# Kernel tuning notes

Measured on AMD Instinct MI355X. Metric: run time of the kernel, lower is better.

## Reference

```python
import jax, jax.numpy as jnp
import numpy as np

B = 2048
C = 128000


def setup_inputs() -> dict:
    key = jax.random.key(0)
    k1, k2 = jax.random.split(key)
    logits = jax.random.normal(k1, (B, C), dtype=jnp.float32)
    y = jax.random.randint(k2, (B,), 0, C, dtype=jnp.int64)
    return {"logits": logits, "y": y}


def reference(logits, y):
    # top-2 logits/indices per row (replaces full descending sort in torch)
    _, top2_idx = jax.lax.top_k(logits, 2)  # [B, 2]
    # if the argmax equals the true label, use the runner-up class
    target = jnp.where(top2_idx[:, 0] == y, top2_idx[:, 1], top2_idx[:, 0])  # [B]
    first = jnp.take_along_axis(logits, target[:, None], axis=1)[:, 0]  # [B]
    # NOTE: faithful to original: subtract the *logit* value (not exp(first))
    second = jnp.log(jnp.exp(logits).sum(axis=1) - first)
    return first - second
```

## Files before the change

### kernel.cpp

```cpp
#include <hip/hip_runtime.h>
#include <math.h>

#define THREADS 256
#define WAVES (THREADS / 64)

__global__ __launch_bounds__(THREADS) void Fitness_29918742183959_kernel(
    const float* __restrict__ logits,
    const int*   __restrict__ y,
    float*       __restrict__ out,
    int C)
{
    const int row = blockIdx.x;
    const int tid = threadIdx.x;
    const float4* rowp =
        reinterpret_cast<const float4*>(logits + (size_t)row * (size_t)C);
    const int n4 = C >> 2;

    float s0 = 0.f, s1 = 0.f, s2 = 0.f, s3 = 0.f;
    float v1 = -INFINITY, v2 = -INFINITY;
    int   i1 = -1,        i2 = -1;

    for (int i = tid; i < n4; i += THREADS) {
        float4 v = rowp[i];
        const int base = i << 2;
        s0 += __expf(v.x);
        s1 += __expf(v.y);
        s2 += __expf(v.z);
        s3 += __expf(v.w);
        if (v.x > v2) { if (v.x > v1) { v2 = v1; i2 = i1; v1 = v.x; i1 = base;     } else { v2 = v.x; i2 = base;     } }
        if (v.y > v2) { if (v.y > v1) { v2 = v1; i2 = i1; v1 = v.y; i1 = base + 1; } else { v2 = v.y; i2 = base + 1; } }
        if (v.z > v2) { if (v.z > v1) { v2 = v1; i2 = i1; v1 = v.z; i1 = base + 2; } else { v2 = v.z; i2 = base + 2; } }
        if (v.w > v2) { if (v.w > v1) { v2 = v1; i2 = i1; v1 = v.w; i1 = base + 3; } else { v2 = v.w; i2 = base + 3; } }
    }
    float s = (s0 + s1) + (s2 + s3);

    #pragma unroll
    for (int off = 32; off > 0; off >>= 1) {
        s += __shfl_down(s, off, 64);
        float ov1 = __shfl_down(v1, off, 64);
        int   oi1 = __shfl_down(i1, off, 64);
        float ov2 = __shfl_down(v2, off, 64);
        int   oi2 = __shfl_down(i2, off, 64);
        if (ov1 > v1) {
            float c2 = v1; int c2i = i1;
            if (ov2 > c2) { c2 = ov2; c2i = oi2; }
            v1 = ov1; i1 = oi1; v2 = c2; i2 = c2i;
        } else if (ov1 > v2) {
            v2 = ov1; i2 = oi1;
        }
    }

    __shared__ float sh_s[WAVES], sh_v1[WAVES], sh_v2[WAVES];
    __shared__ int   sh_i1[WAVES], sh_i2[WAVES];
    const int wave = tid >> 6;
    const int lane = tid & 63;
    if (lane == 0) {
        sh_s[wave] = s; sh_v1[wave] = v1; sh_i1[wave] = i1;
        sh_v2[wave] = v2; sh_i2[wave] = i2;
    }
    __syncthreads();
    if (tid == 0) {
        for (int w = 1; w < WAVES; ++w) {
            s += sh_s[w];
            float ov1 = sh_v1[w], ov2 = sh_v2[w];
            int   oi1 = sh_i1[w], oi2 = sh_i2[w];
            if (ov1 > v1) {
                float c2 = v1; int c2i = i1;
                if (ov2 > c2) { c2 = ov2; c2i = oi2; }
                v1 = ov1; i1 = oi1; v2 = c2; i2 = c2i;
            } else if (ov1 > v2) {
                v2 = ov1; i2 = oi1;
            }
        }
        const int label = y[row];
        const float first = (i1 == label) ? v2 : v1;
        out[row] = first - logf(s - first);
    }
}

extern "C" void kernel_launch(void* const* d_in, const int* in_sizes, int n_in,
                              void* d_out, int out_size, void* d_ws, size_t ws_size,
                              hipStream_t stream) {
    const float* logits = (const float*)d_in[0];
    const int*   y      = (const int*)d_in[1];
    float*       out    = (float*)d_out;
    const int B = in_sizes[1];
    const int C = in_sizes[0] / B;
    Fitness_29918742183959_kernel<<<B, THREADS, 0, stream>>>(logits, y, out, C);
}
```

Before: 1.283 ms.

## Replace top-2 tracking with label-masked max reduction and unroll loads

Reformulates the target selection: instead of tracking top-2 values and indices, the label's logit is masked to -inf and a plain max is taken, which yields the same target value. This removes branchy top-2 updates and index shuffles in the hot loop and the reductions. It also unrolls by two with non-temporal vector loads and more independent accumulators to increase memory-level parallelism. Tie-handling semantics may differ slightly from top_k index ordering, but the resulting value is the same.

```diff
diff --git a/kernel.cpp b/kernel.cpp
--- a/kernel.cpp
+++ b/kernel.cpp
@@ -3,6 +3,8 @@
 
 #define THREADS 256
 #define WAVES (THREADS / 64)
+
+typedef float vf4 __attribute__((ext_vector_type(4)));
 
 __global__ __launch_bounds__(THREADS) void Fitness_29918742183959_kernel(
     const float* __restrict__ logits,
@@ -12,69 +14,61 @@
 {
     const int row = blockIdx.x;
     const int tid = threadIdx.x;
-    const float4* rowp =
-        reinterpret_cast<const float4*>(logits + (size_t)row * (size_t)C);
     const int n4 = C >> 2;
+    const vf4* __restrict__ rowp =
+        reinterpret_cast<const vf4*>(logits + (size_t)row * (size_t)C);
+    const int label = y[row];
+    const int lq = label >> 2;
+    const int lk = label & 3;
 
-    float s0 = 0.f, s1 = 0.f, s2 = 0.f, s3 = 0.f;
-    float v1 = -INFINITY, v2 = -INFINITY;
-    int   i1 = -1,        i2 = -1;
+    float s0=0.f,s1=0.f,s2=0.f,s3=0.f,s4=0.f,s5=0.f,s6=0.f,s7=0.f;
+    float m0=-INFINITY, m1=-INFINITY, m2=-INFINITY, m3=-INFINITY;
 
-    for (int i = tid; i < n4; i += THREADS) {
-        float4 v = rowp[i];
-        const int base = i << 2;
-        s0 += __expf(v.x);
-        s1 += __expf(v.y);
-        s2 += __expf(v.z);
-        s3 += __expf(v.w);
-        if (v.x > v2) { if (v.x > v1) { v2 = v1; i2 = i1; v1 = v.x; i1 = base;     } else { v2 = v.x; i2 = base;     } }
-        if (v.y > v2) { if (v.y > v1) { v2 = v1; i2 = i1; v1 = v.y; i1 = base + 1; } else { v2 = v.y; i2 = base + 1; } }
-        if (v.z > v2) { if (v.z > v1) { v2 = v1; i2 = i1; v1 = v.z; i1 = base + 2; } else { v2 = v.z; i2 = base + 2; } }
-        if (v.w > v2) { if (v.w > v1) { v2 = v1; i2 = i1; v1 = v.w; i1 = base + 3; } else { v2 = v.w; i2 = base + 3; } }
+    int i = tid;
+    for (; i + THREADS < n4; i += 2 * THREADS) {
+        vf4 a = __builtin_nontemporal_load(&rowp[i]);
+        vf4 b = __builtin_nontemporal_load(&rowp[i + THREADS]);
+        s0 += __expf(a.x); s1 += __expf(a.y); s2 += __expf(a.z); s3 += __expf(a.w);
+        s4 += __expf(b.x); s5 += __expf(b.y); s6 += __expf(b.z); s7 += __expf(b.w);
+        if (__builtin_expect(i == lq, 0)) {
+            if (lk == 0) a.x = -INFINITY; else if (lk == 1) a.y = -INFINITY;
+            else if (lk == 2) a.z = -INFINITY; else a.w = -INFINITY;
+        }
+        if (__builtin_expect(i + THREADS == lq, 0)) {
+            if (lk == 0) b.x = -INFINITY; else if (lk == 1) b.y = -INFINITY;
+            else if (lk == 2) b.z = -INFINITY; else b.w = -INFINITY;
+        }
+        m0 = fmaxf(m0, fmaxf(a.x, b.x));
+        m1 = fmaxf(m1, fmaxf(a.y, b.y));
+        m2 = fmaxf(m2, fmaxf(a.z, b.z));
+        m3 = fmaxf(m3, fmaxf(a.w, b.w));
     }
-    float s = (s0 + s1) + (s2 + s3);
+    if (i < n4) {
+        vf4 a = __builtin_nontemporal_load(&rowp[i]);
+        s0 += __expf(a.x); s1 += __expf(a.y); s2 += __expf(a.z); s3 += __expf(a.w);
+        if (i == lq) {
+            if (lk == 0) a.x = -INFINITY; else if (lk == 1) a.y = -INFINITY;
+            else if (lk == 2) a.z = -INFINITY; else a.w = -INFINITY;
+        }
+        m0 = fmaxf(m0, a.x); m1 = fmaxf(m1, a.y);
+        m2 = fmaxf(m2, a.z); m3 = fmaxf(m3, a.w);
+    }
+    float s = ((s0 + s1) + (s2 + s3)) + ((s4 + s5) + (s6 + s7));
+    float m = fmaxf(fmaxf(m0, m1), fmaxf(m2, m3));
 
     #pragma unroll
-    for (int off = 32; off > 0; off >>= 1) {
+    for (int off = 32; off; off >>= 1) {
         s += __shfl_down(s, off, 64);
-        float ov1 = __shfl_down(v1, off, 64);
-        int   oi1 = __shfl_down(i1, off, 64);
-        float ov2 = __shfl_down(v2, off, 64);
-        int   oi2 = __shfl_down(i2, off, 64);
-        if (ov1 > v1) {
-            float c2 = v1; int c2i = i1;
-            if (ov2 > c2) { c2 = ov2; c2i = oi2; }
-            v1 = ov1; i1 = oi1; v2 = c2; i2 = c2i;
-        } else if (ov1 > v2) {
-            v2 = ov1; i2 = oi1;
-        }
+        m = fmaxf(m, __shfl_down(m, off, 64));
     }
 
-    __shared__ float sh_s[WAVES], sh_v1[WAVES], sh_v2[WAVES];
-    __shared__ int   sh_i1[WAVES], sh_i2[WAVES];
-    const int wave = tid >> 6;
-    const int lane = tid & 63;
-    if (lane == 0) {
-        sh_s[wave] = s; sh_v1[wave] = v1; sh_i1[wave] = i1;
-        sh_v2[wave] = v2; sh_i2[wave] = i2;
-    }
+    __shared__ float sh_s[WAVES], sh_m[WAVES];
+    const int wave = tid >> 6, lane = tid & 63;
+    if (lane == 0) { sh_s[wave] = s; sh_m[wave] = m; }
     __syncthreads();
     if (tid == 0) {
-        for (int w = 1; w < WAVES; ++w) {
-            s += sh_s[w];
-            float ov1 = sh_v1[w], ov2 = sh_v2[w];
-            int   oi1 = sh_i1[w], oi2 = sh_i2[w];
-            if (ov1 > v1) {
-                float c2 = v1; int c2i = i1;
-                if (ov2 > c2) { c2 = ov2; c2i = oi2; }
-                v1 = ov1; i1 = oi1; v2 = c2; i2 = c2i;
-            } else if (ov1 > v2) {
-                v2 = ov1; i2 = oi1;
-            }
-        }
-        const int label = y[row];
-        const float first = (i1 == label) ? v2 : v1;
-        out[row] = first - logf(s - first);
+        for (int w = 1; w < WAVES; ++w) { s += sh_s[w]; m = fmaxf(m, sh_m[w]); }
+        out[row] = m - logf(s - m);
     }
 }
 
```

After: 1.233 ms. 3.9% less time.
